# Kernel optimization log

Measured on AMD Instinct MI355X. Metric: run time of the kernel, lower is better.

The kernel has to match this reference:

```python
import jax, jax.numpy as jnp
import numpy as np

N, E, D, H, C = 100000, 1600000, 64, 64, 16


def setup_inputs() -> dict:
    key = jax.random.key(0)
    ks = jax.random.split(key, 8)
    x = jax.random.normal(ks[0], (N, D), dtype=jnp.float32)
    edge_index = jax.random.randint(ks[1], (2, E), 0, N, dtype=jnp.int64)
    W1 = jax.random.normal(ks[2], (D, H), dtype=jnp.float32) * (1.0 / np.sqrt(D))
    b1 = jax.random.normal(ks[3], (H,), dtype=jnp.float32) * 0.01
    W2 = jax.random.normal(ks[4], (H, H), dtype=jnp.float32) * (1.0 / np.sqrt(H))
    b2 = jax.random.normal(ks[5], (H,), dtype=jnp.float32) * 0.01
    Wl = jax.random.normal(ks[6], (H, C), dtype=jnp.float32) * (1.0 / np.sqrt(H))
    bl = jax.random.normal(ks[7], (C,), dtype=jnp.float32) * 0.01
    return {"x": x, "edge_index": edge_index, "W1": W1, "b1": b1,
            "W2": W2, "b2": b2, "Wl": Wl, "bl": bl}


def reference(x, edge_index, W1, b1, W2, b2, Wl, bl):
    n = x.shape[0]
    src, dst = edge_index[0], edge_index[1]
    # GCN symmetric normalization with self-loops: deg = 1 + in-degree at dst
    deg = jax.ops.segment_sum(jnp.ones(src.shape[0], x.dtype), dst, num_segments=n) + 1.0
    inv = jax.lax.rsqrt(deg)                      # deg^{-1/2}, [N]
    norm_e = inv[src] * inv[dst]                  # per-edge norm, [E]
    self_w = inv * inv                            # self-loop weight deg^{-1}, [N]

    def gcn(h, W, b):
        h = h @ W                                 # linear transform first (PyG GCNConv)
        agg = jax.ops.segment_sum(h[src] * norm_e[:, None], dst, num_segments=n)
        agg = agg + h * self_w[:, None]           # self-loop contribution
        return agg + b

    h = jax.nn.relu(gcn(x, W1, b1))
    h = jax.nn.relu(gcn(h, W2, b2))
    return h @ Wl + bl
```

## Files before the change

### kernel.cpp

```cpp
#include <hip/hip_runtime.h>
#include <hip/hip_fp16.h>


#define WS_ALIGN 256
#define BSHIFT 8
#define MAXBUCK 512

typedef _Float16 half8 __attribute__((ext_vector_type(8)));
typedef float floatx4 __attribute__((ext_vector_type(4)));


__global__ void k_bhist(const int* __restrict__ dst, int* __restrict__ bhist,
                        int e, int nbuck) {
    __shared__ int hist[MAXBUCK];
    const int CH = 4096;
    int base = blockIdx.x * CH;
    int end = base + CH; if (end > e) end = e;
    for (int t = threadIdx.x; t < nbuck; t += blockDim.x) hist[t] = 0;
    __syncthreads();
    for (int i = base + threadIdx.x; i < end; i += blockDim.x)
        atomicAdd(&hist[dst[i] >> BSHIFT], 1);
    __syncthreads();
    for (int t = threadIdx.x; t < nbuck; t += blockDim.x)
        if (hist[t]) atomicAdd(&bhist[t], hist[t]);
}

__global__ void k_bscan(const int* __restrict__ bhist, int* __restrict__ gbase,
                        int* __restrict__ gcursor, int e, int nbuck) {
    __shared__ int tmp[MAXBUCK];
    int t = threadIdx.x;
    int v = (t < nbuck) ? bhist[t] : 0;
    tmp[t] = v;
    __syncthreads();
    int x = v;
    #pragma unroll
    for (int d = 1; d < MAXBUCK; d <<= 1) {
        int y = (t >= d) ? tmp[t - d] : 0;
        __syncthreads();
        x += y;
        tmp[t] = x;
        __syncthreads();
    }
    if (t < nbuck) { gbase[t] = x - v; gcursor[t] = x - v; }
    if (t == 0) gbase[nbuck] = e;
}

__global__ void k_partition(const int* __restrict__ src, const int* __restrict__ dst,
                            int* __restrict__ gcursor, int* __restrict__ bpairs,
                            int e, int nbuck) {
    __shared__ int hist[MAXBUCK];
    __shared__ int lbase[MAXBUCK];
    const int CH = 4096;
    int base = blockIdx.x * CH;
    int end = base + CH; if (end > e) end = e;
    for (int t = threadIdx.x; t < nbuck; t += blockDim.x) hist[t] = 0;
    __syncthreads();
    for (int i = base + threadIdx.x; i < end; i += blockDim.x)
        atomicAdd(&hist[dst[i] >> BSHIFT], 1);
    __syncthreads();
    for (int t = threadIdx.x; t < nbuck; t += blockDim.x) {
        int c = hist[t];
        lbase[t] = (c > 0) ? atomicAdd(&gcursor[t], c) : 0;
        hist[t] = 0;
    }
    __syncthreads();
    for (int i = base + threadIdx.x; i < end; i += blockDim.x) {
        int s = src[i], d = dst[i];
        int b = d >> BSHIFT;
        int p = lbase[b] + atomicAdd(&hist[b], 1);
        bpairs[p] = (s << BSHIFT) | (d & ((1 << BSHIFT) - 1));
    }
}

__global__ void k_bfin(const int* __restrict__ bpairs, const int* __restrict__ gbase,
                       int2* __restrict__ ocnt, float* __restrict__ inv,
                       int* __restrict__ ssrc, int n) {
    __shared__ int lcnt[256];
    __shared__ int tmp[256];
    __shared__ int loff[256];
    __shared__ int lcur[256];
    const int b = blockIdx.x;
    const int t = threadIdx.x;
    const int lo = gbase[b];
    const int hi = gbase[b + 1];
    lcnt[t] = 0; lcur[t] = 0;
    __syncthreads();
    for (int i = lo + t; i < hi; i += 256)
        atomicAdd(&lcnt[bpairs[i] & 255], 1);
    __syncthreads();
    int v = lcnt[t];
    tmp[t] = v;
    __syncthreads();
    int x = v;
    #pragma unroll
    for (int d = 1; d < 256; d <<= 1) {
        int y = (t >= d) ? tmp[t - d] : 0;
        __syncthreads();
        x += y;
        tmp[t] = x;
        __syncthreads();
    }
    loff[t] = x - v;
    int node = (b << BSHIFT) + t;
    if (node < n) {
        ocnt[node] = make_int2(lo + (x - v), v);
        inv[node] = rsqrtf((float)v + 1.0f);
    }
    __syncthreads();
    for (int i = lo + t; i < hi; i += 256) {
        int p = bpairs[i];
        int l = p & 255;
        int pos = lo + loff[l] + atomicAdd(&lcur[l], 1);
        ssrc[pos] = p >> BSHIFT;
    }
}


__device__ __forceinline__ void loadA(const float* in, size_t base, half8& a) {
    float4 lo = *reinterpret_cast<const float4*>(in + base);
    float4 hi = *reinterpret_cast<const float4*>(in + base + 16);
    a[0] = (_Float16)lo.x; a[1] = (_Float16)lo.y; a[2] = (_Float16)lo.z; a[3] = (_Float16)lo.w;
    a[4] = (_Float16)hi.x; a[5] = (_Float16)hi.y; a[6] = (_Float16)hi.z; a[7] = (_Float16)hi.w;
}
__device__ __forceinline__ void loadA(const __half* in, size_t base, half8& a) {
    const _Float16* p = reinterpret_cast<const _Float16*>(in + base);
    #pragma unroll
    for (int j = 0; j < 4; ++j) { a[j] = p[j]; a[4 + j] = p[16 + j]; }
}

template <typename Tin>
__global__ void __launch_bounds__(256, 4)
k_transform(const Tin* __restrict__ in, const float* __restrict__ W,
            const float* __restrict__ inv, __half* __restrict__ out, int n) {
    const int lane = threadIdx.x & 63;
    const int m = lane & 15, g = lane >> 4;
    const int wid = blockIdx.x * 4 + (threadIdx.x >> 6);
    const int nw = gridDim.x * 4;

    half8 bf[4][2];
    #pragma unroll
    for (int t = 0; t < 4; ++t)
        #pragma unroll
        for (int s = 0; s < 2; ++s) {
            #pragma unroll
            for (int j = 0; j < 4; ++j) {
                bf[t][s][j]     = (_Float16)W[(32 * s + 4 * g + j) * 64 + 16 * t + m];
                bf[t][s][4 + j] = (_Float16)W[(32 * s + 16 + 4 * g + j) * 64 + 16 * t + m];
            }
        }

    const int ntile = (n + 15) >> 4;
    for (int tile = wid; tile < ntile; tile += nw) {
        const int rbase = tile << 4;
        int arow = rbase + m; if (arow >= n) arow = n - 1;
        half8 a[2];
        loadA(in, (size_t)arow * 64 + 0  + 4 * g, a[0]);
        loadA(in, (size_t)arow * 64 + 32 + 4 * g, a[1]);

        floatx4 acc[4] = {{0.f,0.f,0.f,0.f},{0.f,0.f,0.f,0.f},{0.f,0.f,0.f,0.f},{0.f,0.f,0.f,0.f}};
        #pragma unroll
        for (int s = 0; s < 2; ++s)
            #pragma unroll
            for (int t = 0; t < 4; ++t)
                acc[t] = __builtin_amdgcn_mfma_f32_16x16x32_f16(a[s], bf[t][s], acc[t], 0, 0, 0);

        #pragma unroll
        for (int reg = 0; reg < 4; ++reg) {
            int row = rbase + 4 * g + reg;
            if (row < n) {
                float iv = inv[row];
                #pragma unroll
                for (int t = 0; t < 4; ++t)
                    out[(size_t)row * 64 + 16 * t + m] = __float2half(acc[t][reg] * iv);
            }
        }
    }
}


__global__ void __launch_bounds__(256, 8)
k_aggregate(const __half* __restrict__ t, const int* __restrict__ ssrc,
            const int2* __restrict__ ocnt, const float* __restrict__ inv,
            const float* __restrict__ b, __half* __restrict__ out,
            int n, int do_relu) {
    const int lane = threadIdx.x & 63;
    const int g = lane >> 3;
    const int f = lane & 7;
    const int wid = blockIdx.x * (blockDim.x >> 6) + (threadIdx.x >> 6);
    const int nw = gridDim.x * (blockDim.x >> 6);
    float b8[8];
    #pragma unroll
    for (int q = 0; q < 8; ++q) b8[q] = b[f * 8 + q];

    for (int node = wid; node < n; node += nw) {
        const int2 oc = ocnt[node];
        const int start = oc.x, cnt = oc.y;
        const int tot = cnt + 1;
        float acc[8] = {0.f,0.f,0.f,0.f,0.f,0.f,0.f,0.f};
        for (int be = 0; be < tot; be += 64) {
            int lim = tot - be; if (lim > 64) lim = 64;
            int myidx = (be + lane < cnt) ? ssrc[start + be + lane] : node;
            for (int j = 0; j < lim; j += 8) {
                int epos = j + g;
                int sidx = __shfl(myidx, epos);
                float wt = (epos < lim) ? 1.f : 0.f;
                float4 raw = *reinterpret_cast<const float4*>(t + (size_t)sidx * 64 + f * 8);
                const __half2* hp = reinterpret_cast<const __half2*>(&raw);
                #pragma unroll
                for (int q = 0; q < 4; ++q) {
                    float2 fv = __half22float2(hp[q]);
                    acc[2 * q]     = fmaf(fv.x, wt, acc[2 * q]);
                    acc[2 * q + 1] = fmaf(fv.y, wt, acc[2 * q + 1]);
                }
            }
        }
        #pragma unroll
        for (int off = 8; off < 64; off <<= 1)
            #pragma unroll
            for (int q = 0; q < 8; ++q)
                acc[q] += __shfl_xor(acc[q], off);
        if (g == 0) {
            const float iv = inv[node];
            __half hres[8];
            #pragma unroll
            for (int q = 0; q < 8; ++q) {
                float r = fmaf(acc[q], iv, b8[q]);
                if (do_relu) r = fmaxf(r, 0.f);
                hres[q] = __float2half(r);
            }
            *reinterpret_cast<float4*>(out + (size_t)node * 64 + f * 8) =
                *reinterpret_cast<const float4*>(hres);
        }
    }
}


__global__ void k_final(const __half* __restrict__ h, const float* __restrict__ Wl,
                        const float* __restrict__ bl, float* __restrict__ out, int n) {
    __shared__ float Ws[64 * 16];
    for (int i = threadIdx.x; i < 64 * 16; i += blockDim.x) Ws[i] = Wl[i];
    __syncthreads();
    const int lane = threadIdx.x & 63;
    const int r = lane >> 4, c = lane & 15;
    const int wid = blockIdx.x * (blockDim.x >> 6) + (threadIdx.x >> 6);
    const int nw = gridDim.x * (blockDim.x >> 6);
    const float blc = bl[c];
    for (int base = wid * 4; base < n; base += nw * 4) {
        int row = base + r;
        if (row < n) {
            float acc = blc;
            const __half* hrow = h + (size_t)row * 64;
            #pragma unroll
            for (int kk = 0; kk < 8; ++kk) {
                float4 raw = *reinterpret_cast<const float4*>(hrow + kk * 8);
                const __half2* hp = reinterpret_cast<const __half2*>(&raw);
                #pragma unroll
                for (int j = 0; j < 4; ++j) {
                    float2 fv = __half22float2(hp[j]);
                    acc = fmaf(fv.x, Ws[(kk * 8 + 2 * j + 0) * 16 + c],
                          fmaf(fv.y, Ws[(kk * 8 + 2 * j + 1) * 16 + c], acc));
                }
            }
            out[(size_t)row * 16 + c] = acc;
        }
    }
}


extern "C" void kernel_launch(void* const* d_in, const int* in_sizes, int n_in,
                              void* d_out, int out_size, void* d_ws, size_t ws_size,
                              hipStream_t stream) {
    const float* x  = (const float*)d_in[0];
    const int*   ei = (const int*)d_in[1];
    const float* W1 = (const float*)d_in[2];
    const float* b1 = (const float*)d_in[3];
    const float* W2 = (const float*)d_in[4];
    const float* b2 = (const float*)d_in[5];
    const float* Wl = (const float*)d_in[6];
    const float* bl = (const float*)d_in[7];
    float* out = (float*)d_out;

    const int n = in_sizes[0] / 64;
    const int e = in_sizes[1] / 2;
    const int* src = ei;
    const int* dst = ei + e;
    const int nbuck = (n + (1 << BSHIFT) - 1) >> BSHIFT;
    const int nchunk = (e + 4095) / 4096;

    char* ws = (char*)d_ws;
    size_t off = 0;
    auto alloc = [&](size_t bytes) -> void* {
        void* p = ws + off;
        off += (bytes + (WS_ALIGN - 1)) & ~((size_t)WS_ALIGN - 1);
        return p;
    };
    int*    bhist   = (int*)alloc((size_t)MAXBUCK * 4);
    int*    gbase   = (int*)alloc((size_t)(MAXBUCK + 1) * 4);
    int*    gcursor = (int*)alloc((size_t)MAXBUCK * 4);
    int2*   ocnt    = (int2*)alloc((size_t)n * 8);
    float*  inv     = (float*)alloc((size_t)n * 4);
    int*    ssrc    = (int*)alloc((size_t)e * 4);
    __half* bufA    = (__half*)alloc((size_t)n * 64 * 2);
    __half* bufB    = (__half*)alloc((size_t)n * 64 * 2);
    int*    bpairs  = (int*)bufA;

    hipMemsetAsync(bhist, 0, (size_t)MAXBUCK * 4, stream);

    k_bhist<<<nchunk, 256, 0, stream>>>(dst, bhist, e, nbuck);
    k_bscan<<<1, MAXBUCK, 0, stream>>>(bhist, gbase, gcursor, e, nbuck);
    k_partition<<<nchunk, 256, 0, stream>>>(src, dst, gcursor, bpairs, e, nbuck);
    k_bfin<<<nbuck, 256, 0, stream>>>(bpairs, gbase, ocnt, inv, ssrc, n);

    const int ntile = (n + 15) / 16;
    const int tgrid = (ntile + 3) / 4;
    k_transform<float><<<tgrid, 256, 0, stream>>>(x, W1, inv, bufA, n);
    k_aggregate<<<2048, 256, 0, stream>>>(bufA, ssrc, ocnt, inv, b1, bufB, n, 1);
    k_transform<__half><<<tgrid, 256, 0, stream>>>(bufB, W2, inv, bufA, n);
    k_aggregate<<<2048, 256, 0, stream>>>(bufA, ssrc, ocnt, inv, b2, bufB, n, 1);
    k_final<<<2048, 256, 0, stream>>>(bufB, Wl, bl, out, n);
}
```

Measured before the change: 181.8 us.

## Drop histogram pass via fixed-capacity buckets and fuse final linear into aggregation

The separate bucket-histogram kernel and its scan are removed. Partition now writes into fixed-capacity per-bucket regions (CAP slots each), sends overflow entries to a spill list, and the scan runs on the resulting counts. The final linear layer is fused into the second aggregate kernel through shuffle reductions, which removes k_final and the write and re-read of the hidden buffer. It also prefetches the next node's offset and count. In exchange, a large spill scanned by every bucket block could cost a lot, and the fused epilogue adds register pressure.

```diff
diff --git a/kernel.cpp b/kernel.cpp
--- a/kernel.cpp
+++ b/kernel.cpp
@@ -5,48 +5,15 @@
 #define WS_ALIGN 256
 #define BSHIFT 8
 #define MAXBUCK 512
+#define CAP 6144
 
 typedef _Float16 half8 __attribute__((ext_vector_type(8)));
 typedef float floatx4 __attribute__((ext_vector_type(4)));
 
 
-__global__ void k_bhist(const int* __restrict__ dst, int* __restrict__ bhist,
-                        int e, int nbuck) {
-    __shared__ int hist[MAXBUCK];
-    const int CH = 4096;
-    int base = blockIdx.x * CH;
-    int end = base + CH; if (end > e) end = e;
-    for (int t = threadIdx.x; t < nbuck; t += blockDim.x) hist[t] = 0;
-    __syncthreads();
-    for (int i = base + threadIdx.x; i < end; i += blockDim.x)
-        atomicAdd(&hist[dst[i] >> BSHIFT], 1);
-    __syncthreads();
-    for (int t = threadIdx.x; t < nbuck; t += blockDim.x)
-        if (hist[t]) atomicAdd(&bhist[t], hist[t]);
-}
-
-__global__ void k_bscan(const int* __restrict__ bhist, int* __restrict__ gbase,
-                        int* __restrict__ gcursor, int e, int nbuck) {
-    __shared__ int tmp[MAXBUCK];
-    int t = threadIdx.x;
-    int v = (t < nbuck) ? bhist[t] : 0;
-    tmp[t] = v;
-    __syncthreads();
-    int x = v;
-    #pragma unroll
-    for (int d = 1; d < MAXBUCK; d <<= 1) {
-        int y = (t >= d) ? tmp[t - d] : 0;
-        __syncthreads();
-        x += y;
-        tmp[t] = x;
-        __syncthreads();
-    }
-    if (t < nbuck) { gbase[t] = x - v; gcursor[t] = x - v; }
-    if (t == 0) gbase[nbuck] = e;
-}
-
 __global__ void k_partition(const int* __restrict__ src, const int* __restrict__ dst,
-                            int* __restrict__ gcursor, int* __restrict__ bpairs,
+                            int* __restrict__ gcursor, int* __restrict__ spillcnt,
+                            int* __restrict__ bpairs, int2* __restrict__ spill,
                             int e, int nbuck) {
     __shared__ int hist[MAXBUCK];
     __shared__ int lbase[MAXBUCK];
@@ -67,26 +34,56 @@
     for (int i = base + threadIdx.x; i < end; i += blockDim.x) {
         int s = src[i], d = dst[i];
         int b = d >> BSHIFT;
-        int p = lbase[b] + atomicAdd(&hist[b], 1);
-        bpairs[p] = (s << BSHIFT) | (d & ((1 << BSHIFT) - 1));
-    }
-}
-
-__global__ void k_bfin(const int* __restrict__ bpairs, const int* __restrict__ gbase,
-                       int2* __restrict__ ocnt, float* __restrict__ inv,
-                       int* __restrict__ ssrc, int n) {
+        int pos = lbase[b] + atomicAdd(&hist[b], 1);
+        int packed = (s << BSHIFT) | (d & ((1 << BSHIFT) - 1));
+        if (pos < CAP) bpairs[b * CAP + pos] = packed;
+        else { int si = atomicAdd(spillcnt, 1); spill[si] = make_int2(b, packed); }
+    }
+}
+
+__global__ void k_bscan(const int* __restrict__ gcursor, int* __restrict__ gbase,
+                        int e, int nbuck) {
+    __shared__ int tmp[MAXBUCK];
+    int t = threadIdx.x;
+    int v = (t < nbuck) ? gcursor[t] : 0;
+    tmp[t] = v;
+    __syncthreads();
+    int x = v;
+    #pragma unroll
+    for (int d = 1; d < MAXBUCK; d <<= 1) {
+        int y = (t >= d) ? tmp[t - d] : 0;
+        __syncthreads();
+        x += y;
+        tmp[t] = x;
+        __syncthreads();
+    }
+    if (t < nbuck) gbase[t] = x - v;
+    if (t == 0) gbase[nbuck] = e;
+}
+
+__global__ void k_bfin(const int* __restrict__ bpairs, const int* __restrict__ gcursor,
+                       const int* __restrict__ gbase, const int* __restrict__ spillcnt,
+                       const int2* __restrict__ spill, int2* __restrict__ ocnt,
+                       float* __restrict__ inv, int* __restrict__ ssrc, int n) {
     __shared__ int lcnt[256];
     __shared__ int tmp[256];
     __shared__ int loff[256];
     __shared__ int lcur[256];
     const int b = blockIdx.x;
     const int t = threadIdx.x;
+    const int tot = gcursor[b];
+    const int reg = (tot < CAP) ? tot : CAP;
+    const int rb = b * CAP;
     const int lo = gbase[b];
-    const int hi = gbase[b + 1];
+    const int spn = *spillcnt;
     lcnt[t] = 0; lcur[t] = 0;
     __syncthreads();
-    for (int i = lo + t; i < hi; i += 256)
-        atomicAdd(&lcnt[bpairs[i] & 255], 1);
+    for (int i = t; i < reg; i += 256)
+        atomicAdd(&lcnt[bpairs[rb + i] & 255], 1);
+    for (int i = t; i < spn; i += 256) {
+        int2 sp = spill[i];
+        if (sp.x == b) atomicAdd(&lcnt[sp.y & 255], 1);
+    }
     __syncthreads();
     int v = lcnt[t];
     tmp[t] = v;
@@ -107,11 +104,19 @@
         inv[node] = rsqrtf((float)v + 1.0f);
     }
     __syncthreads();
-    for (int i = lo + t; i < hi; i += 256) {
-        int p = bpairs[i];
+    for (int i = t; i < reg; i += 256) {
+        int p = bpairs[rb + i];
         int l = p & 255;
         int pos = lo + loff[l] + atomicAdd(&lcur[l], 1);
         ssrc[pos] = p >> BSHIFT;
+    }
+    for (int i = t; i < spn; i += 256) {
+        int2 sp = spill[i];
+        if (sp.x == b) {
+            int l = sp.y & 255;
+            int pos = lo + loff[l] + atomicAdd(&lcur[l], 1);
+            ssrc[pos] = sp.y >> BSHIFT;
+        }
     }
 }
 
@@ -178,11 +183,13 @@
 }
 
 
+template <int FINAL>
 __global__ void __launch_bounds__(256, 8)
 k_aggregate(const __half* __restrict__ t, const int* __restrict__ ssrc,
             const int2* __restrict__ ocnt, const float* __restrict__ inv,
-            const float* __restrict__ b, __half* __restrict__ out,
-            int n, int do_relu) {
+            const float* __restrict__ b, const float* __restrict__ Wl,
+            const float* __restrict__ bl, __half* __restrict__ outH,
+            float* __restrict__ outF, int n) {
     const int lane = threadIdx.x & 63;
     const int g = lane >> 3;
     const int f = lane & 7;
@@ -191,10 +198,23 @@
     float b8[8];
     #pragma unroll
     for (int q = 0; q < 8; ++q) b8[q] = b[f * 8 + q];
-
+    float wl0[8], wl1[8];
+    float2 bl2 = make_float2(0.f, 0.f);
+    if (FINAL) {
+        #pragma unroll
+        for (int q = 0; q < 8; ++q) {
+            wl0[q] = Wl[(f * 8 + q) * 16 + 2 * g];
+            wl1[q] = Wl[(f * 8 + q) * 16 + 2 * g + 1];
+        }
+        bl2 = make_float2(bl[2 * g], bl[2 * g + 1]);
+    }
+
+    if (wid >= n) return;
+    int2 oc = ocnt[wid];
     for (int node = wid; node < n; node += nw) {
-        const int2 oc = ocnt[node];
         const int start = oc.x, cnt = oc.y;
+        const int nn = node + nw;
+        if (nn < n) oc = ocnt[nn];
         const int tot = cnt + 1;
         float acc[8] = {0.f,0.f,0.f,0.f,0.f,0.f,0.f,0.f};
         for (int be = 0; be < tot; be += 64) {
@@ -219,49 +239,35 @@
             #pragma unroll
             for (int q = 0; q < 8; ++q)
                 acc[q] += __shfl_xor(acc[q], off);
-        if (g == 0) {
-            const float iv = inv[node];
-            __half hres[8];
+        const float iv = inv[node];
+        if (!FINAL) {
+            if (g == 0) {
+                __half hres[8];
+                #pragma unroll
+                for (int q = 0; q < 8; ++q) {
+                    float r = fmaxf(fmaf(acc[q], iv, b8[q]), 0.f);
+                    hres[q] = __float2half(r);
+                }
+                *reinterpret_cast<float4*>(outH + (size_t)node * 64 + f * 8) =
+                    *reinterpret_cast<const float4*>(hres);
+            }
+        } else {
+            float res[8];
+            #pragma unroll
+            for (int q = 0; q < 8; ++q)
+                res[q] = fmaxf(fmaf(acc[q], iv, b8[q]), 0.f);
+            float p0 = 0.f, p1 = 0.f;
             #pragma unroll
             for (int q = 0; q < 8; ++q) {
-                float r = fmaf(acc[q], iv, b8[q]);
-                if (do_relu) r = fmaxf(r, 0.f);
-                hres[q] = __float2half(r);
-            }
-            *reinterpret_cast<float4*>(out + (size_t)node * 64 + f * 8) =
-                *reinterpret_cast<const float4*>(hres);
-        }
-    }
-}
-
-
-__global__ void k_final(const __half* __restrict__ h, const float* __restrict__ Wl,
-                        const float* __restrict__ bl, float* __restrict__ out, int n) {
-    __shared__ float Ws[64 * 16];
-    for (int i = threadIdx.x; i < 64 * 16; i += blockDim.x) Ws[i] = Wl[i];
-    __syncthreads();
-    const int lane = threadIdx.x & 63;
-    const int r = lane >> 4, c = lane & 15;
-    const int wid = blockIdx.x * (blockDim.x >> 6) + (threadIdx.x >> 6);
-    const int nw = gridDim.x * (blockDim.x >> 6);
-    const float blc = bl[c];
-    for (int base = wid * 4; base < n; base += nw * 4) {
-        int row = base + r;
-        if (row < n) {
-            float acc = blc;
-            const __half* hrow = h + (size_t)row * 64;
-            #pragma unroll
-            for (int kk = 0; kk < 8; ++kk) {
-                float4 raw = *reinterpret_cast<const float4*>(hrow + kk * 8);
-                const __half2* hp = reinterpret_cast<const __half2*>(&raw);
-                #pragma unroll
-                for (int j = 0; j < 4; ++j) {
-                    float2 fv = __half22float2(hp[j]);
-                    acc = fmaf(fv.x, Ws[(kk * 8 + 2 * j + 0) * 16 + c],
-                          fmaf(fv.y, Ws[(kk * 8 + 2 * j + 1) * 16 + c], acc));
-                }
-            }
-            out[(size_t)row * 16 + c] = acc;
+                p0 = fmaf(res[q], wl0[q], p0);
+                p1 = fmaf(res[q], wl1[q], p1);
+            }
+            p0 += __shfl_xor(p0, 1); p0 += __shfl_xor(p0, 2); p0 += __shfl_xor(p0, 4);
+            p1 += __shfl_xor(p1, 1); p1 += __shfl_xor(p1, 2); p1 += __shfl_xor(p1, 4);
+            if (f == 0) {
+                float2 o = make_float2(p0 + bl2.x, p1 + bl2.y);
+                *reinterpret_cast<float2*>(outF + (size_t)node * 16 + 2 * g) = o;
+            }
         }
     }
 }
@@ -294,28 +300,27 @@
         off += (bytes + (WS_ALIGN - 1)) & ~((size_t)WS_ALIGN - 1);
         return p;
     };
-    int*    bhist   = (int*)alloc((size_t)MAXBUCK * 4);
+    int*    gcursor = (int*)alloc((size_t)(MAXBUCK + 1) * 4);
     int*    gbase   = (int*)alloc((size_t)(MAXBUCK + 1) * 4);
-    int*    gcursor = (int*)alloc((size_t)MAXBUCK * 4);
     int2*   ocnt    = (int2*)alloc((size_t)n * 8);
     float*  inv     = (float*)alloc((size_t)n * 4);
     int*    ssrc    = (int*)alloc((size_t)e * 4);
     __half* bufA    = (__half*)alloc((size_t)n * 64 * 2);
     __half* bufB    = (__half*)alloc((size_t)n * 64 * 2);
     int*    bpairs  = (int*)bufA;
-
-    hipMemsetAsync(bhist, 0, (size_t)MAXBUCK * 4, stream);
-
-    k_bhist<<<nchunk, 256, 0, stream>>>(dst, bhist, e, nbuck);
-    k_bscan<<<1, MAXBUCK, 0, stream>>>(bhist, gbase, gcursor, e, nbuck);
-    k_partition<<<nchunk, 256, 0, stream>>>(src, dst, gcursor, bpairs, e, nbuck);
-    k_bfin<<<nbuck, 256, 0, stream>>>(bpairs, gbase, ocnt, inv, ssrc, n);
+    int2*   spill   = (int2*)bufB;
+    int*    spillcnt = gcursor + MAXBUCK;
+
+    hipMemsetAsync(gcursor, 0, (size_t)(MAXBUCK + 1) * 4, stream);
+
+    k_partition<<<nchunk, 256, 0, stream>>>(src, dst, gcursor, spillcnt, bpairs, spill, e, nbuck);
+    k_bscan<<<1, MAXBUCK, 0, stream>>>(gcursor, gbase, e, nbuck);
+    k_bfin<<<nbuck, 256, 0, stream>>>(bpairs, gcursor, gbase, spillcnt, spill, ocnt, inv, ssrc, n);
 
     const int ntile = (n + 15) / 16;
     const int tgrid = (ntile + 3) / 4;
     k_transform<float><<<tgrid, 256, 0, stream>>>(x, W1, inv, bufA, n);
-    k_aggregate<<<2048, 256, 0, stream>>>(bufA, ssrc, ocnt, inv, b1, bufB, n, 1);
+    k_aggregate<0><<<2048, 256, 0, stream>>>(bufA, ssrc, ocnt, inv, b1, Wl, bl, bufB, out, n);
     k_transform<__half><<<tgrid, 256, 0, stream>>>(bufB, W2, inv, bufA, n);
-    k_aggregate<<<2048, 256, 0, stream>>>(bufA, ssrc, ocnt, inv, b2, bufB, n, 1);
-    k_final<<<2048, 256, 0, stream>>>(bufB, Wl, bl, out, n);
-}
+    k_aggregate<1><<<2048, 256, 0, stream>>>(bufA, ssrc, ocnt, inv, b2, Wl, bl, bufB, out, n);
+}
```

Result: no change. 178.3 us (-1.9%).
